# Optimization experiments

Measured on AMD Instinct MI355X. Metric: run time of the kernel, lower is better.

## Reference

```python
import jax, jax.numpy as jnp
import numpy as np

WEIGHT = 0.15  # APPR residual constant (constructor arg `weight`)
N_NODES = 100000
D_FEAT = 64
N_EDGES = 1600000


def setup_inputs() -> dict:
    key = jax.random.key(0)
    kx, ke = jax.random.split(key)
    x = jax.random.normal(kx, (N_NODES, D_FEAT), dtype=jnp.float32)
    edge_index = jax.random.randint(ke, (2, N_EDGES), 0, N_NODES, dtype=jnp.int64)
    return {"x": x, "edge_index": edge_index}


def reference(x, edge_index):
    # PyG flow='source_to_target': message x_j = x[edge_index[0]],
    # scatter-add onto destination nodes edge_index[1].
    src = edge_index[0]
    dst = edge_index[1]
    aggr = jax.ops.segment_sum(x[src], dst, num_segments=x.shape[0])  # [N, D]
    return x + WEIGHT * aggr
```

## Files before the change

kernel.cpp:

```cpp
#include <hip/hip_runtime.h>
#include <hip/hip_bf16.h>

#define APPR_WEIGHT 0.15f
#define D_FEAT 64
#define BUCKET_BITS 8
#define BUCKET_NODES 256
#define MAX_NB 512
#define SCAT_THREADS 512
#define SCAT_EPT 8
#define SCAT_EPB (SCAT_THREADS * SCAT_EPT)
#define CSR_BUF 8192
#define BCAP 5120

typedef float f32x4 __attribute__((ext_vector_type(4)));

__global__ void appr_copy_kernel(const float4* __restrict__ x,
                                 float4* __restrict__ out, int n4) {
    int i = blockIdx.x * blockDim.x + threadIdx.x;
    if (i < n4) out[i] = x[i];
}

__global__ void appr_scatter_kernel(const float* __restrict__ x,
                                    const int* __restrict__ src,
                                    const int* __restrict__ dst,
                                    float* __restrict__ out,
                                    int n_edges) {
    long long idx = (long long)blockIdx.x * blockDim.x + threadIdx.x;
    long long total = (long long)n_edges * D_FEAT;
    if (idx >= total) return;
    int e = (int)(idx >> 6);
    int f = (int)(idx & 63);
    float v = APPR_WEIGHT * x[(long long)src[e] * D_FEAT + f];
    unsafeAtomicAdd(&out[(long long)dst[e] * D_FEAT + f], v);
}

__global__ void bucket_scatter_kernel(const int* __restrict__ src,
                                      const int* __restrict__ dst,
                                      int* __restrict__ cursor,
                                      unsigned int* __restrict__ grouped,
                                      int n_edges, int nb) {
    __shared__ unsigned int staged[SCAT_EPB];
    __shared__ int hist[MAX_NB];
    __shared__ int lexcl[MAX_NB];
    __shared__ int gbase[MAX_NB];
    __shared__ int lcur[MAX_NB];
    int tid = threadIdx.x;
    for (int i = tid; i < nb; i += SCAT_THREADS) { hist[i] = 0; lcur[i] = 0; }
    __syncthreads();

    long long base = (long long)blockIdx.x * SCAT_EPB;
    int mysrc[SCAT_EPT];
    int mydst[SCAT_EPT];
#pragma unroll
    for (int k = 0; k < SCAT_EPT; ++k) {
        long long e = base + (long long)k * SCAT_THREADS + tid;
        if (e < n_edges) {
            mysrc[k] = src[e];
            mydst[k] = dst[e];
            atomicAdd(&hist[mydst[k] >> BUCKET_BITS], 1);
        } else {
            mydst[k] = -1;
        }
    }
    __syncthreads();

    int hv = (tid < MAX_NB) ? hist[tid] : 0;
    if (tid < MAX_NB) lexcl[tid] = hv;
    __syncthreads();
    for (int off = 1; off < MAX_NB; off <<= 1) {
        int t = (tid < MAX_NB && tid >= off) ? lexcl[tid - off] : 0;
        __syncthreads();
        if (tid < MAX_NB) lexcl[tid] += t;
        __syncthreads();
    }
    if (tid < MAX_NB) lexcl[tid] -= hv;
    if (tid < nb) gbase[tid] = hv ? atomicAdd(&cursor[tid], hv) : 0;
    __syncthreads();

#pragma unroll
    for (int k = 0; k < SCAT_EPT; ++k) {
        if (mydst[k] >= 0) {
            int b = mydst[k] >> BUCKET_BITS;
            int r = atomicAdd(&lcur[b], 1);
            staged[lexcl[b] + r] =
                ((unsigned)mysrc[k] << BUCKET_BITS) |
                (unsigned)(mydst[k] & (BUCKET_NODES - 1));
        }
    }
    __syncthreads();

    int wave = tid >> 6;
    int lane = tid & 63;
    int nwaves = SCAT_THREADS >> 6;
    for (int b = wave; b < nb; b += nwaves) {
        int cnt = hist[b];
        int lb = lexcl[b];
        int gb = gbase[b];
        for (int j = lane; j < cnt; j += 64)
            grouped[gb + j] = staged[lb + j];
    }
}


__global__ void convert_bf16_kernel(const float4* __restrict__ x4,
                                    uint4* __restrict__ xhp, int n8,
                                    int* __restrict__ cursor, int nb) {
    if (blockIdx.x == 0)
        for (int b = threadIdx.x; b < nb; b += blockDim.x) cursor[b] = b * BCAP;
    int i = blockIdx.x * blockDim.x + threadIdx.x;
    if (i >= n8) return;
    float4 a = x4[2 * i];
    float4 b = x4[2 * i + 1];
    __hip_bfloat16 h0 = __float2bfloat16(a.x), h1 = __float2bfloat16(a.y);
    __hip_bfloat16 h2 = __float2bfloat16(a.z), h3 = __float2bfloat16(a.w);
    __hip_bfloat16 h4 = __float2bfloat16(b.x), h5 = __float2bfloat16(b.y);
    __hip_bfloat16 h6 = __float2bfloat16(b.z), h7 = __float2bfloat16(b.w);
    uint4 o;
    o.x = (unsigned)*(unsigned short*)&h0 | ((unsigned)*(unsigned short*)&h1 << 16);
    o.y = (unsigned)*(unsigned short*)&h2 | ((unsigned)*(unsigned short*)&h3 << 16);
    o.z = (unsigned)*(unsigned short*)&h4 | ((unsigned)*(unsigned short*)&h5 << 16);
    o.w = (unsigned)*(unsigned short*)&h6 | ((unsigned)*(unsigned short*)&h7 << 16);
    xhp[i] = o;
}

__global__ void csr_build_fixed_kernel(unsigned int* grouped,
                                       const int* __restrict__ cursor,
                                       int* __restrict__ node_beg,
                                       int* __restrict__ node_end,
                                       int n_nodes) {
    __shared__ unsigned int buf[BCAP];
    __shared__ unsigned int buf2[BCAP];
    __shared__ int hist[BUCKET_NODES];
    __shared__ int excl[BUCKET_NODES];
    __shared__ int cur[BUCKET_NODES];
    int tid = threadIdx.x;
    int b = blockIdx.x;
    int beg = b * BCAP;
    int cnt = cursor[b] - beg;
    if (cnt > BCAP) cnt = BCAP;

    if (tid < BUCKET_NODES) hist[tid] = 0;
    __syncthreads();
    for (int i = tid; i < cnt; i += blockDim.x) {
        unsigned int w = grouped[beg + i];
        buf[i] = w;
        atomicAdd(&hist[w & (BUCKET_NODES - 1)], 1);
    }
    __syncthreads();
    int v = (tid < BUCKET_NODES) ? hist[tid] : 0;
    if (tid < BUCKET_NODES) excl[tid] = v;
    __syncthreads();
    for (int off = 1; off < BUCKET_NODES; off <<= 1) {
        int t = (tid < BUCKET_NODES && tid >= off) ? excl[tid - off] : 0;
        __syncthreads();
        if (tid < BUCKET_NODES) excl[tid] += t;
        __syncthreads();
    }
    if (tid < BUCKET_NODES) {
        int e = excl[tid] - v;
        cur[tid] = e;
        int node = (b << BUCKET_BITS) + tid;
        if (node < n_nodes) {
            node_beg[node] = beg + e;
            node_end[node] = beg + e + v;
        }
    }
    __syncthreads();
    for (int i = tid; i < cnt; i += blockDim.x) {
        unsigned int w = buf[i];
        int pos = atomicAdd(&cur[w & (BUCKET_NODES - 1)], 1);
        buf2[pos] = w >> BUCKET_BITS;
    }
    __syncthreads();
    for (int i = tid; i < cnt; i += blockDim.x)
        grouped[beg + i] = buf2[i];
}

__global__ void csr_aggregate_bf16_kernel(const uint4* __restrict__ xhp,
                                          const float4* __restrict__ x4,
                                          const int* __restrict__ node_beg,
                                          const int* __restrict__ node_end,
                                          const unsigned int* __restrict__ srcs,
                                          float4* __restrict__ out4,
                                          int n_nodes) {
    int gid = blockIdx.x * blockDim.x + threadIdx.x;
    int node = gid >> 5;
    if (node >= n_nodes) return;
    int l32 = threadIdx.x & 31;
    int sub = l32 >> 3;
    int q = l32 & 7;

    int nbeg = node_beg[node];
    int nend = node_end[node];

    float acc[8] = {0.f, 0.f, 0.f, 0.f, 0.f, 0.f, 0.f, 0.f};
    for (int e0 = nbeg; e0 < nend; e0 += 16) {
#pragma unroll
        for (int u = 0; u < 4; ++u) {
            int i = e0 + u * 4 + sub;
            if (i < nend) {
                int s = (int)srcs[i];
                uint4 h = xhp[s * 8 + q];
                acc[0] += __uint_as_float(h.x << 16);
                acc[1] += __uint_as_float(h.x & 0xffff0000u);
                acc[2] += __uint_as_float(h.y << 16);
                acc[3] += __uint_as_float(h.y & 0xffff0000u);
                acc[4] += __uint_as_float(h.z << 16);
                acc[5] += __uint_as_float(h.z & 0xffff0000u);
                acc[6] += __uint_as_float(h.w << 16);
                acc[7] += __uint_as_float(h.w & 0xffff0000u);
            }
        }
    }
#pragma unroll
    for (int k = 0; k < 8; ++k) {
        acc[k] += __shfl_xor(acc[k], 8, 64);
        acc[k] += __shfl_xor(acc[k], 16, 64);
    }

    if (sub == 0) {
        float4 xv0 = x4[node * 16 + q * 2];
        float4 xv1 = x4[node * 16 + q * 2 + 1];
        f32x4 o0, o1;
        o0.x = xv0.x + APPR_WEIGHT * acc[0];
        o0.y = xv0.y + APPR_WEIGHT * acc[1];
        o0.z = xv0.z + APPR_WEIGHT * acc[2];
        o0.w = xv0.w + APPR_WEIGHT * acc[3];
        o1.x = xv1.x + APPR_WEIGHT * acc[4];
        o1.y = xv1.y + APPR_WEIGHT * acc[5];
        o1.z = xv1.z + APPR_WEIGHT * acc[6];
        o1.w = xv1.w + APPR_WEIGHT * acc[7];
        __builtin_nontemporal_store(o0, (f32x4*)&out4[node * 16 + q * 2]);
        __builtin_nontemporal_store(o1, (f32x4*)&out4[node * 16 + q * 2 + 1]);
    }
}


__global__ void bucket_hist_kernel(const int* __restrict__ dst,
                                   int* __restrict__ bcount,
                                   int n_edges, int nb) {
    __shared__ int h[MAX_NB];
    for (int i = threadIdx.x; i < nb; i += blockDim.x) h[i] = 0;
    __syncthreads();
    for (long long e = blockIdx.x * (long long)blockDim.x + threadIdx.x;
         e < n_edges; e += (long long)gridDim.x * blockDim.x) {
        atomicAdd(&h[dst[e] >> BUCKET_BITS], 1);
    }
    __syncthreads();
    for (int i = threadIdx.x; i < nb; i += blockDim.x)
        if (h[i]) atomicAdd(&bcount[i], h[i]);
}

__global__ void bucket_scan_kernel(const int* __restrict__ bcount,
                                   int* __restrict__ boff,
                                   int* __restrict__ cursor, int nb) {
    __shared__ int lds[MAX_NB];
    int tid = threadIdx.x;
    int v = (tid < nb) ? bcount[tid] : 0;
    lds[tid] = v;
    __syncthreads();
    for (int off = 1; off < MAX_NB; off <<= 1) {
        int t = (tid >= off) ? lds[tid - off] : 0;
        __syncthreads();
        lds[tid] += t;
        __syncthreads();
    }
    if (tid < nb) {
        int excl = lds[tid] - v;
        boff[tid] = excl;
        cursor[tid] = excl;
    }
    if (tid == nb - 1) boff[nb] = lds[tid];
}

__global__ void csr_build_kernel(unsigned int* grouped,
                                 const int* __restrict__ boff,
                                 int* __restrict__ node_off,
                                 int n_nodes, int nb) {
    __shared__ unsigned int buf[CSR_BUF];
    __shared__ int hist[BUCKET_NODES];
    __shared__ int excl[BUCKET_NODES];
    __shared__ int cur[BUCKET_NODES];
    int tid = threadIdx.x;
    int b = blockIdx.x;
    int beg = boff[b];
    int end = boff[b + 1];
    int cnt = end - beg;
    if (cnt > CSR_BUF) cnt = CSR_BUF;

    if (tid < BUCKET_NODES) hist[tid] = 0;
    __syncthreads();
    for (int i = tid; i < cnt; i += blockDim.x) {
        unsigned int w = grouped[beg + i];
        buf[i] = w;
        atomicAdd(&hist[w & (BUCKET_NODES - 1)], 1);
    }
    __syncthreads();
    int v = (tid < BUCKET_NODES) ? hist[tid] : 0;
    if (tid < BUCKET_NODES) excl[tid] = v;
    __syncthreads();
    for (int off = 1; off < BUCKET_NODES; off <<= 1) {
        int t = (tid < BUCKET_NODES && tid >= off) ? excl[tid - off] : 0;
        __syncthreads();
        if (tid < BUCKET_NODES) excl[tid] += t;
        __syncthreads();
    }
    if (tid < BUCKET_NODES) {
        int e = excl[tid] - v;
        cur[tid] = e;
        int node = (b << BUCKET_BITS) + tid;
        if (node < n_nodes) node_off[node] = beg + e;
    }
    if (b == nb - 1 && tid == 0) node_off[n_nodes] = end;
    __syncthreads();
    for (int i = tid; i < cnt; i += blockDim.x) {
        unsigned int w = buf[i];
        int pos = atomicAdd(&cur[w & (BUCKET_NODES - 1)], 1);
        grouped[beg + pos] = w >> BUCKET_BITS;
    }
}

__global__ void csr_aggregate_kernel(const float4* __restrict__ x4,
                                     const int* __restrict__ node_off,
                                     const unsigned int* __restrict__ srcs,
                                     float4* __restrict__ out4,
                                     int n_nodes) {
    int gid = blockIdx.x * blockDim.x + threadIdx.x;
    int node = gid >> 6;
    if (node >= n_nodes) return;
    int lane = threadIdx.x & 63;
    int sub = lane >> 4;
    int q = lane & 15;

    int nbeg = node_off[node];
    int nend = node_off[node + 1];

    float4 acc = make_float4(0.f, 0.f, 0.f, 0.f);
    for (int e0 = nbeg; e0 < nend; e0 += 16) {
#pragma unroll
        for (int u = 0; u < 4; ++u) {
            int i = e0 + u * 4 + sub;
            if (i < nend) {
                int s = (int)srcs[i];
                float4 vv = x4[s * (D_FEAT / 4) + q];
                acc.x += vv.x; acc.y += vv.y; acc.z += vv.z; acc.w += vv.w;
            }
        }
    }
    acc.x += __shfl_xor(acc.x, 16, 64);
    acc.y += __shfl_xor(acc.y, 16, 64);
    acc.z += __shfl_xor(acc.z, 16, 64);
    acc.w += __shfl_xor(acc.w, 16, 64);
    acc.x += __shfl_xor(acc.x, 32, 64);
    acc.y += __shfl_xor(acc.y, 32, 64);
    acc.z += __shfl_xor(acc.z, 32, 64);
    acc.w += __shfl_xor(acc.w, 32, 64);

    if (lane < 16) {
        float4 xv = x4[node * (D_FEAT / 4) + q];
        float4 o;
        o.x = xv.x + APPR_WEIGHT * acc.x;
        o.y = xv.y + APPR_WEIGHT * acc.y;
        o.z = xv.z + APPR_WEIGHT * acc.z;
        o.w = xv.w + APPR_WEIGHT * acc.w;
        out4[node * (D_FEAT / 4) + q] = o;
    }
}

extern "C" void kernel_launch(void* const* d_in, const int* in_sizes, int n_in,
                              void* d_out, int out_size, void* d_ws, size_t ws_size,
                              hipStream_t stream) {
    const float* x = (const float*)d_in[0];
    const int* edge_index = (const int*)d_in[1];
    float* out = (float*)d_out;

    int n_feat_total = in_sizes[0];
    int n_nodes = n_feat_total / D_FEAT;
    int n_edges = in_sizes[1] / 2;

    const int* src = edge_index;
    const int* dst = edge_index + n_edges;

    int nb = (n_nodes + BUCKET_NODES - 1) >> BUCKET_BITS;
    int sg = (n_edges + SCAT_EPB - 1) / SCAT_EPB;

    float meanb = (float)n_edges / (float)nb;
    bool cap_ok = (meanb + 12.0f * sqrtf(meanb)) <= (float)BCAP;
    size_t need_primary = (size_t)(MAX_NB + 2 * n_nodes + (size_t)nb * BCAP) * 4
                          + (size_t)n_feat_total * 2;
    if (nb <= MAX_NB && cap_ok && ws_size >= need_primary) {
        int* cursor           = (int*)d_ws;
        int* node_beg         = cursor + MAX_NB;
        int* node_end         = node_beg + n_nodes;
        unsigned int* grouped = (unsigned int*)(node_end + n_nodes);
        uint4* xhp            = (uint4*)(grouped + (size_t)nb * BCAP);

        int n8 = n_feat_total / 8;
        convert_bf16_kernel<<<(n8 + 255) / 256, 256, 0, stream>>>(
            (const float4*)x, xhp, n8, cursor, nb);
        bucket_scatter_kernel<<<sg, SCAT_THREADS, 0, stream>>>(
            src, dst, cursor, grouped, n_edges, nb);
        csr_build_fixed_kernel<<<nb, 1024, 0, stream>>>(
            grouped, cursor, node_beg, node_end, n_nodes);
        long long threads = (long long)n_nodes * 32;
        csr_aggregate_bf16_kernel<<<(int)((threads + 255) / 256), 256, 0, stream>>>(
            xhp, (const float4*)x, node_beg, node_end,
            grouped, (float4*)out, n_nodes);
        return;
    }

    size_t need_dense = (size_t)(3 * MAX_NB + 1 + n_edges + n_nodes + 1) * sizeof(int);
    if (nb <= MAX_NB && ws_size >= need_dense) {
        int* bcount           = (int*)d_ws;
        int* boff             = bcount + MAX_NB;
        int* cursor           = boff + (MAX_NB + 1);
        unsigned int* grouped = (unsigned int*)(cursor + MAX_NB);
        int* node_off         = (int*)(grouped + n_edges);

        hipMemsetAsync(bcount, 0, (size_t)MAX_NB * sizeof(int), stream);
        bucket_hist_kernel<<<256, 1024, 0, stream>>>(dst, bcount, n_edges, nb);
        bucket_scan_kernel<<<1, MAX_NB, 0, stream>>>(bcount, boff, cursor, nb);
        bucket_scatter_kernel<<<sg, SCAT_THREADS, 0, stream>>>(
            src, dst, cursor, grouped, n_edges, nb);
        csr_build_kernel<<<nb, 1024, 0, stream>>>(grouped, boff, node_off,
                                                  n_nodes, nb);
        long long threads = (long long)n_nodes * 64;
        csr_aggregate_kernel<<<(int)((threads + 255) / 256), 256, 0, stream>>>(
            (const float4*)x, node_off, grouped, (float4*)out, n_nodes);
        return;
    }

    int n4 = n_feat_total / 4;
    appr_copy_kernel<<<(n4 + 255) / 256, 256, 0, stream>>>(
        (const float4*)x, (float4*)out, n4);
    long long total = (long long)n_edges * D_FEAT;
    appr_scatter_kernel<<<(int)((total + 255) / 256), 256, 0, stream>>>(
        x, src, dst, out, n_edges);
}
```

Before: 151.9 us.

## Fuse bf16 convert into bucket scatter and CSR build into aggregation

Merges the bf16 conversion into the bucket-scatter launch as extra blocks, and fuses the per-bucket CSR construction with neighbor aggregation so sorted source lists stay in LDS. This removes node_beg/node_end arrays, the write-back of sorted sources to global memory, and two kernel launches, replacing cursor initialisation with a memset of per-bucket counts. In exchange the aggregation now runs on only one block per 256-node bucket, reducing parallelism and occupancy for the gather phase.

```diff
diff --git a/kernel.cpp b/kernel.cpp
--- a/kernel.cpp
+++ b/kernel.cpp
@@ -34,6 +34,229 @@
     unsafeAtomicAdd(&out[(long long)dst[e] * D_FEAT + f], v);
 }
 
+__global__ void fused_convert_scatter_kernel(const float4* __restrict__ x4,
+                                             uint4* __restrict__ xhp, int n8,
+                                             const int* __restrict__ src,
+                                             const int* __restrict__ dst,
+                                             int* __restrict__ ccount,
+                                             unsigned int* __restrict__ grouped,
+                                             int n_edges, int nb,
+                                             int n_scat_blocks) {
+    int bid = blockIdx.x;
+    if (bid >= n_scat_blocks) {
+        int i = (bid - n_scat_blocks) * SCAT_THREADS + threadIdx.x;
+        if (i >= n8) return;
+        float4 a = x4[2 * i];
+        float4 b = x4[2 * i + 1];
+        __hip_bfloat16 h0 = __float2bfloat16(a.x), h1 = __float2bfloat16(a.y);
+        __hip_bfloat16 h2 = __float2bfloat16(a.z), h3 = __float2bfloat16(a.w);
+        __hip_bfloat16 h4 = __float2bfloat16(b.x), h5 = __float2bfloat16(b.y);
+        __hip_bfloat16 h6 = __float2bfloat16(b.z), h7 = __float2bfloat16(b.w);
+        uint4 o;
+        o.x = (unsigned)*(unsigned short*)&h0 | ((unsigned)*(unsigned short*)&h1 << 16);
+        o.y = (unsigned)*(unsigned short*)&h2 | ((unsigned)*(unsigned short*)&h3 << 16);
+        o.z = (unsigned)*(unsigned short*)&h4 | ((unsigned)*(unsigned short*)&h5 << 16);
+        o.w = (unsigned)*(unsigned short*)&h6 | ((unsigned)*(unsigned short*)&h7 << 16);
+        xhp[i] = o;
+        return;
+    }
+
+    __shared__ unsigned int staged[SCAT_EPB];
+    __shared__ int hist[MAX_NB];
+    __shared__ int lexcl[MAX_NB];
+    __shared__ int gbase[MAX_NB];
+    __shared__ int lcur[MAX_NB];
+    int tid = threadIdx.x;
+    for (int i = tid; i < nb; i += SCAT_THREADS) { hist[i] = 0; lcur[i] = 0; }
+    __syncthreads();
+
+    long long base = (long long)bid * SCAT_EPB;
+    int mysrc[SCAT_EPT];
+    int mydst[SCAT_EPT];
+#pragma unroll
+    for (int k = 0; k < SCAT_EPT; ++k) {
+        long long e = base + (long long)k * SCAT_THREADS + tid;
+        if (e < n_edges) {
+            mysrc[k] = src[e];
+            mydst[k] = dst[e];
+            atomicAdd(&hist[mydst[k] >> BUCKET_BITS], 1);
+        } else {
+            mydst[k] = -1;
+        }
+    }
+    __syncthreads();
+
+    int hv = (tid < MAX_NB) ? hist[tid] : 0;
+    if (tid < MAX_NB) lexcl[tid] = hv;
+    __syncthreads();
+    for (int off = 1; off < MAX_NB; off <<= 1) {
+        int t = (tid < MAX_NB && tid >= off) ? lexcl[tid - off] : 0;
+        __syncthreads();
+        if (tid < MAX_NB) lexcl[tid] += t;
+        __syncthreads();
+    }
+    if (tid < MAX_NB) lexcl[tid] -= hv;
+    if (tid < nb) gbase[tid] = hv ? (tid * BCAP + atomicAdd(&ccount[tid], hv)) : 0;
+    __syncthreads();
+
+#pragma unroll
+    for (int k = 0; k < SCAT_EPT; ++k) {
+        if (mydst[k] >= 0) {
+            int b = mydst[k] >> BUCKET_BITS;
+            int r = atomicAdd(&lcur[b], 1);
+            staged[lexcl[b] + r] =
+                ((unsigned)mysrc[k] << BUCKET_BITS) |
+                (unsigned)(mydst[k] & (BUCKET_NODES - 1));
+        }
+    }
+    __syncthreads();
+
+    int wave = tid >> 6;
+    int lane = tid & 63;
+    int nwaves = SCAT_THREADS >> 6;
+    for (int b = wave; b < nb; b += nwaves) {
+        int cnt = hist[b];
+        int lb = lexcl[b];
+        int gb = gbase[b];
+        for (int j = lane; j < cnt; j += 64)
+            grouped[gb + j] = staged[lb + j];
+    }
+}
+
+__global__ void fused_build_aggregate_kernel(const uint4* __restrict__ xhp,
+                                             const float4* __restrict__ x4,
+                                             const int* __restrict__ ccount,
+                                             const unsigned int* __restrict__ grouped,
+                                             float4* __restrict__ out4,
+                                             int n_nodes) {
+    __shared__ unsigned int buf[BCAP];
+    __shared__ unsigned int buf2[BCAP];
+    __shared__ int hist[BUCKET_NODES];
+    __shared__ int incl[BUCKET_NODES];
+    __shared__ int cur[BUCKET_NODES];
+    int tid = threadIdx.x;
+    int b = blockIdx.x;
+    int beg = b * BCAP;
+    int cnt = ccount[b];
+    if (cnt > BCAP) cnt = BCAP;
+
+    if (tid < BUCKET_NODES) hist[tid] = 0;
+    __syncthreads();
+    for (int i = tid; i < cnt; i += blockDim.x) {
+        unsigned int w = grouped[beg + i];
+        buf[i] = w;
+        atomicAdd(&hist[w & (BUCKET_NODES - 1)], 1);
+    }
+    __syncthreads();
+    int v = (tid < BUCKET_NODES) ? hist[tid] : 0;
+    if (tid < BUCKET_NODES) incl[tid] = v;
+    __syncthreads();
+    for (int off = 1; off < BUCKET_NODES; off <<= 1) {
+        int t = (tid < BUCKET_NODES && tid >= off) ? incl[tid - off] : 0;
+        __syncthreads();
+        if (tid < BUCKET_NODES) incl[tid] += t;
+        __syncthreads();
+    }
+    if (tid < BUCKET_NODES) cur[tid] = incl[tid] - v;
+    __syncthreads();
+    for (int i = tid; i < cnt; i += blockDim.x) {
+        unsigned int w = buf[i];
+        int pos = atomicAdd(&cur[w & (BUCKET_NODES - 1)], 1);
+        buf2[pos] = w >> BUCKET_BITS;
+    }
+    __syncthreads();
+
+    int g = tid >> 5;
+    int l32 = tid & 31;
+    int sub = l32 >> 3;
+    int q = l32 & 7;
+
+    for (int nloc = g; nloc < BUCKET_NODES; nloc += 32) {
+        int node = (b << BUCKET_BITS) + nloc;
+        if (node >= n_nodes) break;
+        int nend = incl[nloc];
+        int nbeg = nend - hist[nloc];
+
+        float acc[8] = {0.f, 0.f, 0.f, 0.f, 0.f, 0.f, 0.f, 0.f};
+        for (int e0 = nbeg; e0 < nend; e0 += 16) {
+#pragma unroll
+            for (int u = 0; u < 4; ++u) {
+                int i = e0 + u * 4 + sub;
+                if (i < nend) {
+                    int s = (int)buf2[i];
+                    uint4 h = xhp[s * 8 + q];
+                    acc[0] += __uint_as_float(h.x << 16);
+                    acc[1] += __uint_as_float(h.x & 0xffff0000u);
+                    acc[2] += __uint_as_float(h.y << 16);
+                    acc[3] += __uint_as_float(h.y & 0xffff0000u);
+                    acc[4] += __uint_as_float(h.z << 16);
+                    acc[5] += __uint_as_float(h.z & 0xffff0000u);
+                    acc[6] += __uint_as_float(h.w << 16);
+                    acc[7] += __uint_as_float(h.w & 0xffff0000u);
+                }
+            }
+        }
+#pragma unroll
+        for (int k = 0; k < 8; ++k) {
+            acc[k] += __shfl_xor(acc[k], 8, 64);
+            acc[k] += __shfl_xor(acc[k], 16, 64);
+        }
+        if (sub == 0) {
+            float4 xv0 = x4[node * 16 + q * 2];
+            float4 xv1 = x4[node * 16 + q * 2 + 1];
+            f32x4 o0, o1;
+            o0.x = xv0.x + APPR_WEIGHT * acc[0];
+            o0.y = xv0.y + APPR_WEIGHT * acc[1];
+            o0.z = xv0.z + APPR_WEIGHT * acc[2];
+            o0.w = xv0.w + APPR_WEIGHT * acc[3];
+            o1.x = xv1.x + APPR_WEIGHT * acc[4];
+            o1.y = xv1.y + APPR_WEIGHT * acc[5];
+            o1.z = xv1.z + APPR_WEIGHT * acc[6];
+            o1.w = xv1.w + APPR_WEIGHT * acc[7];
+            __builtin_nontemporal_store(o0, (f32x4*)&out4[node * 16 + q * 2]);
+            __builtin_nontemporal_store(o1, (f32x4*)&out4[node * 16 + q * 2 + 1]);
+        }
+    }
+}
+
+
+__global__ void bucket_hist_kernel(const int* __restrict__ dst,
+                                   int* __restrict__ bcount,
+                                   int n_edges, int nb) {
+    __shared__ int h[MAX_NB];
+    for (int i = threadIdx.x; i < nb; i += blockDim.x) h[i] = 0;
+    __syncthreads();
+    for (long long e = blockIdx.x * (long long)blockDim.x + threadIdx.x;
+         e < n_edges; e += (long long)gridDim.x * blockDim.x) {
+        atomicAdd(&h[dst[e] >> BUCKET_BITS], 1);
+    }
+    __syncthreads();
+    for (int i = threadIdx.x; i < nb; i += blockDim.x)
+        if (h[i]) atomicAdd(&bcount[i], h[i]);
+}
+
+__global__ void bucket_scan_kernel(const int* __restrict__ bcount,
+                                   int* __restrict__ boff,
+                                   int* __restrict__ cursor, int nb) {
+    __shared__ int lds[MAX_NB];
+    int tid = threadIdx.x;
+    int v = (tid < nb) ? bcount[tid] : 0;
+    lds[tid] = v;
+    __syncthreads();
+    for (int off = 1; off < MAX_NB; off <<= 1) {
+        int t = (tid >= off) ? lds[tid - off] : 0;
+        __syncthreads();
+        lds[tid] += t;
+        __syncthreads();
+    }
+    if (tid < nb) {
+        int excl = lds[tid] - v;
+        boff[tid] = excl;
+        cursor[tid] = excl;
+    }
+    if (tid == nb - 1) boff[nb] = lds[tid];
+}
+
 __global__ void bucket_scatter_kernel(const int* __restrict__ src,
                                       const int* __restrict__ dst,
                                       int* __restrict__ cursor,
@@ -63,7 +286,6 @@
         }
     }
     __syncthreads();
-
     int hv = (tid < MAX_NB) ? hist[tid] : 0;
     if (tid < MAX_NB) lexcl[tid] = hv;
     __syncthreads();
@@ -76,7 +298,6 @@
     if (tid < MAX_NB) lexcl[tid] -= hv;
     if (tid < nb) gbase[tid] = hv ? atomicAdd(&cursor[tid], hv) : 0;
     __syncthreads();
-
 #pragma unroll
     for (int k = 0; k < SCAT_EPT; ++k) {
         if (mydst[k] >= 0) {
@@ -88,7 +309,6 @@
         }
     }
     __syncthreads();
-
     int wave = tid >> 6;
     int lane = tid & 63;
     int nwaves = SCAT_THREADS >> 6;
@@ -99,178 +319,6 @@
         for (int j = lane; j < cnt; j += 64)
             grouped[gb + j] = staged[lb + j];
     }
-}
-
-
-__global__ void convert_bf16_kernel(const float4* __restrict__ x4,
-                                    uint4* __restrict__ xhp, int n8,
-                                    int* __restrict__ cursor, int nb) {
-    if (blockIdx.x == 0)
-        for (int b = threadIdx.x; b < nb; b += blockDim.x) cursor[b] = b * BCAP;
-    int i = blockIdx.x * blockDim.x + threadIdx.x;
-    if (i >= n8) return;
-    float4 a = x4[2 * i];
-    float4 b = x4[2 * i + 1];
-    __hip_bfloat16 h0 = __float2bfloat16(a.x), h1 = __float2bfloat16(a.y);
-    __hip_bfloat16 h2 = __float2bfloat16(a.z), h3 = __float2bfloat16(a.w);
-    __hip_bfloat16 h4 = __float2bfloat16(b.x), h5 = __float2bfloat16(b.y);
-    __hip_bfloat16 h6 = __float2bfloat16(b.z), h7 = __float2bfloat16(b.w);
-    uint4 o;
-    o.x = (unsigned)*(unsigned short*)&h0 | ((unsigned)*(unsigned short*)&h1 << 16);
-    o.y = (unsigned)*(unsigned short*)&h2 | ((unsigned)*(unsigned short*)&h3 << 16);
-    o.z = (unsigned)*(unsigned short*)&h4 | ((unsigned)*(unsigned short*)&h5 << 16);
-    o.w = (unsigned)*(unsigned short*)&h6 | ((unsigned)*(unsigned short*)&h7 << 16);
-    xhp[i] = o;
-}
-
-__global__ void csr_build_fixed_kernel(unsigned int* grouped,
-                                       const int* __restrict__ cursor,
-                                       int* __restrict__ node_beg,
-                                       int* __restrict__ node_end,
-                                       int n_nodes) {
-    __shared__ unsigned int buf[BCAP];
-    __shared__ unsigned int buf2[BCAP];
-    __shared__ int hist[BUCKET_NODES];
-    __shared__ int excl[BUCKET_NODES];
-    __shared__ int cur[BUCKET_NODES];
-    int tid = threadIdx.x;
-    int b = blockIdx.x;
-    int beg = b * BCAP;
-    int cnt = cursor[b] - beg;
-    if (cnt > BCAP) cnt = BCAP;
-
-    if (tid < BUCKET_NODES) hist[tid] = 0;
-    __syncthreads();
-    for (int i = tid; i < cnt; i += blockDim.x) {
-        unsigned int w = grouped[beg + i];
-        buf[i] = w;
-        atomicAdd(&hist[w & (BUCKET_NODES - 1)], 1);
-    }
-    __syncthreads();
-    int v = (tid < BUCKET_NODES) ? hist[tid] : 0;
-    if (tid < BUCKET_NODES) excl[tid] = v;
-    __syncthreads();
-    for (int off = 1; off < BUCKET_NODES; off <<= 1) {
-        int t = (tid < BUCKET_NODES && tid >= off) ? excl[tid - off] : 0;
-        __syncthreads();
-        if (tid < BUCKET_NODES) excl[tid] += t;
-        __syncthreads();
-    }
-    if (tid < BUCKET_NODES) {
-        int e = excl[tid] - v;
-        cur[tid] = e;
-        int node = (b << BUCKET_BITS) + tid;
-        if (node < n_nodes) {
-            node_beg[node] = beg + e;
-            node_end[node] = beg + e + v;
-        }
-    }
-    __syncthreads();
-    for (int i = tid; i < cnt; i += blockDim.x) {
-        unsigned int w = buf[i];
-        int pos = atomicAdd(&cur[w & (BUCKET_NODES - 1)], 1);
-        buf2[pos] = w >> BUCKET_BITS;
-    }
-    __syncthreads();
-    for (int i = tid; i < cnt; i += blockDim.x)
-        grouped[beg + i] = buf2[i];
-}
-
-__global__ void csr_aggregate_bf16_kernel(const uint4* __restrict__ xhp,
-                                          const float4* __restrict__ x4,
-                                          const int* __restrict__ node_beg,
-                                          const int* __restrict__ node_end,
-                                          const unsigned int* __restrict__ srcs,
-                                          float4* __restrict__ out4,
-                                          int n_nodes) {
-    int gid = blockIdx.x * blockDim.x + threadIdx.x;
-    int node = gid >> 5;
-    if (node >= n_nodes) return;
-    int l32 = threadIdx.x & 31;
-    int sub = l32 >> 3;
-    int q = l32 & 7;
-
-    int nbeg = node_beg[node];
-    int nend = node_end[node];
-
-    float acc[8] = {0.f, 0.f, 0.f, 0.f, 0.f, 0.f, 0.f, 0.f};
-    for (int e0 = nbeg; e0 < nend; e0 += 16) {
-#pragma unroll
-        for (int u = 0; u < 4; ++u) {
-            int i = e0 + u * 4 + sub;
-            if (i < nend) {
-                int s = (int)srcs[i];
-                uint4 h = xhp[s * 8 + q];
-                acc[0] += __uint_as_float(h.x << 16);
-                acc[1] += __uint_as_float(h.x & 0xffff0000u);
-                acc[2] += __uint_as_float(h.y << 16);
-                acc[3] += __uint_as_float(h.y & 0xffff0000u);
-                acc[4] += __uint_as_float(h.z << 16);
-                acc[5] += __uint_as_float(h.z & 0xffff0000u);
-                acc[6] += __uint_as_float(h.w << 16);
-                acc[7] += __uint_as_float(h.w & 0xffff0000u);
-            }
-        }
-    }
-#pragma unroll
-    for (int k = 0; k < 8; ++k) {
-        acc[k] += __shfl_xor(acc[k], 8, 64);
-        acc[k] += __shfl_xor(acc[k], 16, 64);
-    }
-
-    if (sub == 0) {
-        float4 xv0 = x4[node * 16 + q * 2];
-        float4 xv1 = x4[node * 16 + q * 2 + 1];
-        f32x4 o0, o1;
-        o0.x = xv0.x + APPR_WEIGHT * acc[0];
-        o0.y = xv0.y + APPR_WEIGHT * acc[1];
-        o0.z = xv0.z + APPR_WEIGHT * acc[2];
-        o0.w = xv0.w + APPR_WEIGHT * acc[3];
-        o1.x = xv1.x + APPR_WEIGHT * acc[4];
-        o1.y = xv1.y + APPR_WEIGHT * acc[5];
-        o1.z = xv1.z + APPR_WEIGHT * acc[6];
-        o1.w = xv1.w + APPR_WEIGHT * acc[7];
-        __builtin_nontemporal_store(o0, (f32x4*)&out4[node * 16 + q * 2]);
-        __builtin_nontemporal_store(o1, (f32x4*)&out4[node * 16 + q * 2 + 1]);
-    }
-}
-
-
-__global__ void bucket_hist_kernel(const int* __restrict__ dst,
-                                   int* __restrict__ bcount,
-                                   int n_edges, int nb) {
-    __shared__ int h[MAX_NB];
-    for (int i = threadIdx.x; i < nb; i += blockDim.x) h[i] = 0;
-    __syncthreads();
-    for (long long e = blockIdx.x * (long long)blockDim.x + threadIdx.x;
-         e < n_edges; e += (long long)gridDim.x * blockDim.x) {
-        atomicAdd(&h[dst[e] >> BUCKET_BITS], 1);
-    }
-    __syncthreads();
-    for (int i = threadIdx.x; i < nb; i += blockDim.x)
-        if (h[i]) atomicAdd(&bcount[i], h[i]);
-}
-
-__global__ void bucket_scan_kernel(const int* __restrict__ bcount,
-                                   int* __restrict__ boff,
-                                   int* __restrict__ cursor, int nb) {
-    __shared__ int lds[MAX_NB];
-    int tid = threadIdx.x;
-    int v = (tid < nb) ? bcount[tid] : 0;
-    lds[tid] = v;
-    __syncthreads();
-    for (int off = 1; off < MAX_NB; off <<= 1) {
-        int t = (tid >= off) ? lds[tid - off] : 0;
-        __syncthreads();
-        lds[tid] += t;
-        __syncthreads();
-    }
-    if (tid < nb) {
-        int excl = lds[tid] - v;
-        boff[tid] = excl;
-        cursor[tid] = excl;
-    }
-    if (tid == nb - 1) boff[nb] = lds[tid];
 }
 
 __global__ void csr_build_kernel(unsigned int* grouped,
@@ -386,26 +434,22 @@
 
     float meanb = (float)n_edges / (float)nb;
     bool cap_ok = (meanb + 12.0f * sqrtf(meanb)) <= (float)BCAP;
-    size_t need_primary = (size_t)(MAX_NB + 2 * n_nodes + (size_t)nb * BCAP) * 4
+    size_t need_primary = (size_t)(MAX_NB + (size_t)nb * BCAP) * 4
                           + (size_t)n_feat_total * 2;
     if (nb <= MAX_NB && cap_ok && ws_size >= need_primary) {
-        int* cursor           = (int*)d_ws;
-        int* node_beg         = cursor + MAX_NB;
-        int* node_end         = node_beg + n_nodes;
-        unsigned int* grouped = (unsigned int*)(node_end + n_nodes);
+        int* ccount           = (int*)d_ws;
+        unsigned int* grouped = (unsigned int*)(ccount + MAX_NB);
         uint4* xhp            = (uint4*)(grouped + (size_t)nb * BCAP);
 
         int n8 = n_feat_total / 8;
-        convert_bf16_kernel<<<(n8 + 255) / 256, 256, 0, stream>>>(
-            (const float4*)x, xhp, n8, cursor, nb);
-        bucket_scatter_kernel<<<sg, SCAT_THREADS, 0, stream>>>(
-            src, dst, cursor, grouped, n_edges, nb);
-        csr_build_fixed_kernel<<<nb, 1024, 0, stream>>>(
-            grouped, cursor, node_beg, node_end, n_nodes);
-        long long threads = (long long)n_nodes * 32;
-        csr_aggregate_bf16_kernel<<<(int)((threads + 255) / 256), 256, 0, stream>>>(
-            xhp, (const float4*)x, node_beg, node_end,
-            grouped, (float4*)out, n_nodes);
+        int cg = (n8 + SCAT_THREADS - 1) / SCAT_THREADS;
+
+        hipMemsetAsync(ccount, 0, (size_t)MAX_NB * sizeof(int), stream);
+        fused_convert_scatter_kernel<<<sg + cg, SCAT_THREADS, 0, stream>>>(
+            (const float4*)x, xhp, n8, src, dst, ccount, grouped,
+            n_edges, nb, sg);
+        fused_build_aggregate_kernel<<<nb, 1024, 0, stream>>>(
+            xhp, (const float4*)x, ccount, grouped, (float4*)out, n_nodes);
         return;
     }
 
```

After: 140.6 us. -7.4%, faster.
